# Performance work log

Measured on AMD Instinct MI355X. Metric: run time of the kernel, lower is better.

The kernel has to match this reference:

```python
import jax, jax.numpy as jnp
import numpy as np

# Video-DiT scale: d_model = H * D = 2048
B, S_T, S_C, H, D = 2, 2048, 1024, 16, 128


def setup_inputs() -> dict:
    key = jax.random.key(0)
    ks = jax.random.split(key, 6)
    f = lambda k, s: jax.random.normal(k, s, dtype=jnp.float32)
    return {
        "target_q": f(ks[0], (B, S_T, H, D)),
        "target_k": f(ks[1], (B, S_T, H, D)),
        "target_v": f(ks[2], (B, S_T, H, D)),
        "cond_k": f(ks[3], (B, S_C, H, D)),
        "cond_v": f(ks[4], (B, S_C, H, D)),
        "b_param": f(ks[5], (1,)),
    }


def reference(target_q, target_k, target_v, cond_k, cond_v, b_param):
    """Extended target self-attention over [target_k; cond_k] with a scalar
    logit bias b_param added only to the condition-key columns.
    Inputs BSHD; returns [B, S_t, H*D] (ready for output_proj)."""
    Bq, St, Hh, Dd = target_q.shape
    Sc = cond_k.shape[1]
    scale = Dd ** -0.5  # softmax_scale defaults to head_dim**-0.5

    k_ext = jnp.concatenate([target_k, cond_k], axis=1)  # [B, S_t+S_c, H, D]
    v_ext = jnp.concatenate([target_v, cond_v], axis=1)

    # [B, H, S_t, S_t+S_c]
    logits = jnp.einsum('bqhd,bkhd->bhqk', target_q, k_ext) * jnp.asarray(scale, target_q.dtype)
    # bias: 0 on target keys, b on cond keys
    bias = jnp.concatenate([
        jnp.zeros((St,), logits.dtype),
        jnp.broadcast_to(b_param.astype(logits.dtype), (Sc,)),
    ])
    logits = logits + bias[None, None, None, :]

    probs = jax.nn.softmax(logits, axis=-1)
    out = jnp.einsum('bhqk,bkhd->bqhd', probs, v_ext)  # [B, S_t, H, D]
    return out.reshape(Bq, St, Hh * Dd)
```

## Files before the change

### kernel.cpp

```cpp
#include <hip/hip_runtime.h>
#include <hip/hip_bf16.h>

typedef __attribute__((ext_vector_type(4))) float f32x4;
typedef __attribute__((ext_vector_type(16))) float f32x16;
typedef __attribute__((ext_vector_type(8))) short bf8;
typedef __attribute__((ext_vector_type(2))) int i32x2;

#define B_ 2
#define ST 2048
#define SC 1024
#define SK 3072
#define NH 16
#define DH 128
#define KVB 32
#define NT 96
#define TGT 64
#define SCALE 0.088388347648318447f
#define LOG2E 1.4426950408889634f
#define PRE_TILE_U32 2048
#define PRE_BYTES (32ull * 96 * 512 * 16)
#define WS_NEED (2ull * PRE_BYTES)

__device__ __forceinline__ i32x2 tr_read(unsigned a) {
    i32x2 d;
    asm volatile("ds_read_b64_tr_b16 %0, %1" : "=v"(d) : "v"(a));
    return d;
}

__device__ __forceinline__ unsigned cvtpk(float lo, float hi) {
    unsigned r;
    asm("v_cvt_pk_bf16_f32 %0, %1, %2" : "=v"(r) : "v"(lo), "v"(hi));
    return r;
}

__device__ __forceinline__ void swap32(unsigned &a, unsigned &b) {
    asm volatile("v_permlane32_swap_b32 %0, %1" : "+v"(a), "+v"(b));
}

__device__ __forceinline__ bf8 mk_bf8(i32x2 a, i32x2 b) {
    union { i32x2 h[2]; bf8 v; } u;
    u.h[0] = a; u.h[1] = b;
    return u.v;
}
__device__ __forceinline__ bf8 mk_bf8w(unsigned w0, unsigned w1, unsigned w2, unsigned w3) {
    union { unsigned w[4]; bf8 v; } u;
    u.w[0] = w0; u.w[1] = w1; u.w[2] = w2; u.w[3] = w3;
    return u.v;
}
__device__ __forceinline__ bf8 pack_bf8(f32x4 a, f32x4 b) {
    return mk_bf8w(cvtpk(a[0], a[1]), cvtpk(a[2], a[3]),
                   cvtpk(b[0], b[1]), cvtpk(b[2], b[3]));
}

__global__ __launch_bounds__(256)
void preconv(const float* __restrict__ TK, const float* __restrict__ TV,
             const float* __restrict__ CK, const float* __restrict__ CV,
             unsigned* __restrict__ KP, unsigned* __restrict__ VP)
{
    const unsigned gid = blockIdx.x * 256 + threadIdx.x;
    const int c    = gid & 511;
    const int idx  = gid >> 9;
    const int bhid = idx / 96;
    const int t    = idx - bhid * 96;
    const int bb   = bhid >> 4;
    const int hh   = bhid & 15;

    const int krow = c >> 4;
    const int kcol = ((c & 15) ^ (krow & 7)) << 3;
    const int gkv  = t * 32 + krow;
    const float* kp = (gkv < ST)
        ? TK + (((size_t)bb * ST + gkv) * NH + hh) * DH + kcol
        : CK + (((size_t)bb * SC + (gkv - ST)) * NH + hh) * DH + kcol;
    const f32x4 k0 = *(const f32x4*)kp;
    const f32x4 k1 = *(const f32x4*)(kp + 4);
    unsigned* ko = KP + (size_t)gid * 4;
    ko[0] = cvtpk(k0[0], k0[1]); ko[1] = cvtpk(k0[2], k0[3]);
    ko[2] = cvtpk(k1[0], k1[1]); ko[3] = cvtpk(k1[2], k1[3]);

    const int vkv = (((c >> 8) & 1) << 4) | (((c >> 4) & 1) << 3)
                  | (((c >> 7) & 1) << 2) | ((c >> 1) & 3);
    const int vd  = (((c >> 5) & 3) << 5) | (((c >> 3) & 1) << 4)
                  | ((c & 1) << 3);
    const int gvv = t * 32 + vkv;
    const float* vp = (gvv < ST)
        ? TV + (((size_t)bb * ST + gvv) * NH + hh) * DH + vd
        : CV + (((size_t)bb * SC + (gvv - ST)) * NH + hh) * DH + vd;
    const f32x4 v0 = *(const f32x4*)vp;
    const f32x4 v1 = *(const f32x4*)(vp + 4);
    unsigned* vo = VP + (size_t)gid * 4;
    vo[0] = cvtpk(v0[0], v0[1]); vo[1] = cvtpk(v0[2], v0[3]);
    vo[2] = cvtpk(v1[0], v1[1]); vo[3] = cvtpk(v1[2], v1[3]);
}

__global__ __launch_bounds__(256) __attribute__((amdgpu_waves_per_eu(2, 2)))
void attn_fwd_pre(const float* __restrict__ Q,
                  const unsigned* __restrict__ KP,
                  const unsigned* __restrict__ VP,
                  const float* __restrict__ BP,
                  float* __restrict__ OUT)
{
    __shared__ __align__(16) unsigned short Ks[3][KVB * DH];
    __shared__ __align__(16) unsigned short Vs[3][KVB * DH];

    const int tid = threadIdx.x;
    const int w   = tid >> 6;
    const int l   = tid & 63;
    const int r31 = l & 31;
    const int hi  = l >> 5;

    const int bid = blockIdx.x;
    const int xcd = bid & 7;
    const int sub = bid >> 3;
    const int bh  = xcd * 4 + (sub >> 4);
    const int qt  = sub & 15;
    const int bb  = bh >> 4;
    const int hh  = bh & 15;
    const int bh96 = bh * 96;

    const float biasl = BP[0] * LOG2E;

    const int qrow = qt * 128 + w * 32 + r31;
    const float* qp = Q + (((size_t)bb * ST + qrow) * NH + hh) * DH;
    const float qsc = SCALE * LOG2E;
    bf8 qf[8];
#pragma unroll
    for (int dk = 0; dk < 8; ++dk) {
        const f32x4 x0 = *(const f32x4*)(qp + dk * 16 + hi * 8);
        const f32x4 x1 = *(const f32x4*)(qp + dk * 16 + hi * 8 + 4);
        qf[dk] = mk_bf8w(cvtpk(x0[0]*qsc, x0[1]*qsc), cvtpk(x0[2]*qsc, x0[3]*qsc),
                         cvtpk(x1[0]*qsc, x1[1]*qsc), cvtpk(x1[2]*qsc, x1[3]*qsc));
    }

    f32x16 oa[4];
#pragma unroll
    for (int dt = 0; dt < 4; ++dt)
#pragma unroll
        for (int e = 0; e < 16; ++e) oa[dt][e] = 0.f;
    float l_run = 0.f;

    auto stage = [&](int t, int buf) {
        const unsigned* kt = KP + (size_t)(bh96 + t) * PRE_TILE_U32;
        const unsigned* vt = VP + (size_t)(bh96 + t) * PRE_TILE_U32;
#pragma unroll
        for (int i = 0; i < 2; ++i) {
            const int cb = (w << 6) + (i << 8);
            const unsigned kdst = (unsigned)(size_t)&Ks[buf][cb * 8];
            const unsigned vdst = (unsigned)(size_t)&Vs[buf][cb * 8];
            const unsigned* kg = kt + (size_t)(cb + l) * 4;
            const unsigned* vg = vt + (size_t)(cb + l) * 4;
            __builtin_amdgcn_global_load_lds(
                (const __attribute__((address_space(1))) unsigned*)(size_t)kg,
                (__attribute__((address_space(3))) unsigned*)(size_t)kdst, 16, 0, 0);
            __builtin_amdgcn_global_load_lds(
                (const __attribute__((address_space(1))) unsigned*)(size_t)vg,
                (__attribute__((address_space(3))) unsigned*)(size_t)vdst, 16, 0, 0);
        }
    };

    const unsigned vLane = (unsigned)(size_t)&Vs[0][0]
                         + (unsigned)((l >> 4) * 128 + (l & 15) * 8);
    const char* kBase = (const char*)Ks[0];

    auto qk_into = [&](f32x16& SN, int bufn, float biasn) {
#pragma unroll
        for (int e = 0; e < 16; ++e) SN[e] = biasn;
        const char* kB = kBase + (unsigned)bufn * 8192u;
        __builtin_amdgcn_s_setprio(1);
#pragma unroll
        for (int dk = 0; dk < 8; ++dk) {
            int o = r31 * 256 + (dk * 16 + hi * 8) * 2;
            o ^= (r31 & 7) << 4;
            const bf8 kf = *(const bf8*)(kB + o);
            SN = __builtin_amdgcn_mfma_f32_32x32x16_bf16(kf, qf[dk], SN, 0, 0, 0);
        }
        __builtin_amdgcn_s_setprio(0);
    };

    stage(0, 0);
    stage(1, 1);
    asm volatile("s_waitcnt vmcnt(4)" ::: "memory");
    __builtin_amdgcn_s_barrier();
    asm volatile("" ::: "memory");
    f32x16 sA, sB;
    qk_into(sA, 0, 0.f);

    int b0 = 0, b1 = 1, b2 = 2;

    auto body = [&](int t, f32x16& SCr, f32x16& SNr) {
        if (t + 1 < NT) asm volatile("s_waitcnt vmcnt(0)" ::: "memory");
        __builtin_amdgcn_s_barrier();
        asm volatile("" ::: "memory");
        if (t + 2 < NT) stage(t + 2, b2);

        if (t + 1 < NT)
            qk_into(SNr, b1, (t + 1 >= TGT) ? biasl : 0.f);

        const unsigned vA = vLane + (unsigned)b0 * 8192u;
        i32x2 t0_[4][2];
#pragma unroll
        for (int dt = 0; dt < 4; ++dt) {
            t0_[dt][0] = tr_read(vA + dt * 512);
            t0_[dt][1] = tr_read(vA + dt * 512 + 2048);
        }

        float rs = 0.f;
#pragma unroll
        for (int e = 0; e < 16; ++e) {
            SCr[e] = __builtin_amdgcn_exp2f(SCr[e]);
            rs += SCr[e];
        }
        l_run += rs;

        unsigned a0 = cvtpk(SCr[0], SCr[1]),  c0 = cvtpk(SCr[4], SCr[5]);
        unsigned a1 = cvtpk(SCr[2], SCr[3]),  c1 = cvtpk(SCr[6], SCr[7]);
        swap32(a0, c0); swap32(a1, c1);
        const bf8 pf0 = mk_bf8w(a0, a1, c0, c1);
        unsigned a2 = cvtpk(SCr[8], SCr[9]),   c2 = cvtpk(SCr[12], SCr[13]);
        unsigned a3 = cvtpk(SCr[10], SCr[11]), c3 = cvtpk(SCr[14], SCr[15]);
        swap32(a2, c2); swap32(a3, c3);
        const bf8 pf1 = mk_bf8w(a2, a3, c2, c3);

        asm volatile("s_waitcnt lgkmcnt(0)");
        __builtin_amdgcn_sched_barrier(0);
        i32x2 t1_[4][2];
#pragma unroll
        for (int dt = 0; dt < 4; ++dt) {
            t1_[dt][0] = tr_read(vA + 4096 + dt * 512);
            t1_[dt][1] = tr_read(vA + 4096 + dt * 512 + 2048);
        }
        __builtin_amdgcn_s_setprio(1);
#pragma unroll
        for (int dt = 0; dt < 4; ++dt) {
            const bf8 vf = mk_bf8(t0_[dt][0], t0_[dt][1]);
            oa[dt] = __builtin_amdgcn_mfma_f32_32x32x16_bf16(vf, pf0, oa[dt], 0, 0, 0);
        }
        __builtin_amdgcn_s_setprio(0);
        asm volatile("s_waitcnt lgkmcnt(0)");
        __builtin_amdgcn_sched_barrier(0);
        __builtin_amdgcn_s_setprio(1);
#pragma unroll
        for (int dt = 0; dt < 4; ++dt) {
            const bf8 vf = mk_bf8(t1_[dt][0], t1_[dt][1]);
            oa[dt] = __builtin_amdgcn_mfma_f32_32x32x16_bf16(vf, pf1, oa[dt], 0, 0, 0);
        }
        __builtin_amdgcn_s_setprio(0);

        const int n0 = b1, n1 = b2, n2 = b0;
        b0 = n0; b1 = n1; b2 = n2;
    };

    for (int t = 0; t < NT; t += 2) {
        body(t, sA, sB);
        body(t + 1, sB, sA);
    }

    const float l_tot = l_run + __shfl_xor(l_run, 32);
    const float inv = 1.0f / l_tot;
    float* op = OUT + ((size_t)(bb * ST + qrow)) * (NH * DH) + hh * DH;
#pragma unroll
    for (int dt = 0; dt < 4; ++dt)
#pragma unroll
        for (int rr = 0; rr < 4; ++rr) {
            f32x4 st;
            st[0] = oa[dt][rr * 4 + 0] * inv;
            st[1] = oa[dt][rr * 4 + 1] * inv;
            st[2] = oa[dt][rr * 4 + 2] * inv;
            st[3] = oa[dt][rr * 4 + 3] * inv;
            *(f32x4*)(op + dt * 32 + rr * 8 + hi * 4) = st;
        }
}

__global__ __launch_bounds__(256, 2)
void attn_fwd_reg(const float* __restrict__ Q,
                  const float* __restrict__ TK,
                  const float* __restrict__ TV,
                  const float* __restrict__ CK,
                  const float* __restrict__ CV,
                  const float* __restrict__ BP,
                  float* __restrict__ OUT)
{
    __shared__ __align__(16) unsigned short Ks[2][KVB * DH];
    __shared__ __align__(16) unsigned short Vs[2][KVB * DH];

    const int tid = threadIdx.x;
    const int w   = tid >> 6;
    const int l   = tid & 63;
    const int r31 = l & 31;
    const int hi  = l >> 5;

    const int bid = blockIdx.x;
    const int xcd = bid & 7;
    const int sub = bid >> 3;
    const int bh  = xcd * 4 + (sub >> 4);
    const int qt  = sub & 15;
    const int bb  = bh >> 4;
    const int hh  = bh & 15;

    const float biasl = BP[0] * LOG2E;

    const int qrow = qt * 128 + w * 32 + r31;
    const float* qp = Q + (((size_t)bb * ST + qrow) * NH + hh) * DH;
    const float qsc = SCALE * LOG2E;
    bf8 qf[8];
#pragma unroll
    for (int dk = 0; dk < 8; ++dk) {
        const f32x4 x0 = *(const f32x4*)(qp + dk * 16 + hi * 8);
        const f32x4 x1 = *(const f32x4*)(qp + dk * 16 + hi * 8 + 4);
        qf[dk] = mk_bf8w(cvtpk(x0[0]*qsc, x0[1]*qsc), cvtpk(x0[2]*qsc, x0[3]*qsc),
                         cvtpk(x1[0]*qsc, x1[1]*qsc), cvtpk(x1[2]*qsc, x1[3]*qsc));
    }

    f32x16 oa[4];
#pragma unroll
    for (int dt = 0; dt < 4; ++dt)
#pragma unroll
        for (int e = 0; e < 16; ++e) oa[dt][e] = 0.f;
    float l_run = 0.f;

    f32x4 skr[2][2], svr[2][2];

    auto stage_load = [&](int t) {
        const int kv0 = t * KVB;
        const float *kb, *vb;
        if (kv0 < ST) {
            const size_t off = (((size_t)bb * ST + kv0) * NH + hh) * DH;
            kb = TK + off; vb = TV + off;
        } else {
            const size_t off = (((size_t)bb * SC + (kv0 - ST)) * NH + hh) * DH;
            kb = CK + off; vb = CV + off;
        }
#pragma unroll
        for (int i = 0; i < 2; ++i) {
            const int c = tid + (i << 8);
            const int krow = c >> 4;
            const int kcol = ((c & 15) ^ (krow & 7)) << 3;
            const float* kp = kb + (size_t)krow * (NH * DH) + kcol;
            skr[i][0] = *(const f32x4*)kp;
            skr[i][1] = *(const f32x4*)(kp + 4);
            const int vkv = (((c >> 8) & 1) << 4) | (((c >> 4) & 1) << 3)
                          | (((c >> 7) & 1) << 2) | ((c >> 1) & 3);
            const int vd  = (((c >> 5) & 3) << 5) | (((c >> 3) & 1) << 4)
                          | ((c & 1) << 3);
            const float* vp = vb + (size_t)vkv * (NH * DH) + vd;
            svr[i][0] = *(const f32x4*)vp;
            svr[i][1] = *(const f32x4*)(vp + 4);
        }
    };
    auto stage_write = [&](int buf) {
#pragma unroll
        for (int i = 0; i < 2; ++i) {
            const int c = tid + (i << 8);
            *(bf8*)((char*)Ks[buf] + c * 16) = pack_bf8(skr[i][0], skr[i][1]);
            *(bf8*)((char*)Vs[buf] + c * 16) = pack_bf8(svr[i][0], svr[i][1]);
        }
    };

    stage_load(0);
    stage_write(0);

    const unsigned vLane = (unsigned)(size_t)&Vs[0][0]
                         + (unsigned)((l >> 4) * 128 + (l & 15) * 8);

    for (int t = 0; t < NT; ++t) {
        __syncthreads();
        if (t + 1 < NT) stage_load(t + 1);
        const int buf = t & 1;
        const float bias = (t >= TGT) ? biasl : 0.f;

        f32x16 s0;
#pragma unroll
        for (int e = 0; e < 16; ++e) s0[e] = bias;
        __builtin_amdgcn_s_setprio(1);
#pragma unroll
        for (int dk = 0; dk < 8; ++dk) {
            int o = r31 * 256 + (dk * 16 + hi * 8) * 2;
            o ^= (r31 & 7) << 4;
            const bf8 kf = *(const bf8*)((const char*)Ks[buf] + o);
            s0 = __builtin_amdgcn_mfma_f32_32x32x16_bf16(kf, qf[dk], s0, 0, 0, 0);
        }
        __builtin_amdgcn_s_setprio(0);

        asm volatile("" ::: "memory");
        const unsigned vA = vLane + (unsigned)(buf << 13);
        i32x2 vt_[2][4][2];
#pragma unroll
        for (int ks = 0; ks < 2; ++ks) {
            const unsigned vk = vA + (unsigned)(ks << 12);
#pragma unroll
            for (int dt = 0; dt < 4; ++dt) {
                vt_[ks][dt][0] = tr_read(vk + dt * 512);
                vt_[ks][dt][1] = tr_read(vk + dt * 512 + 2048);
            }
        }

        if (t + 1 < NT) stage_write(buf ^ 1);

        float rs = 0.f;
#pragma unroll
        for (int e = 0; e < 16; ++e) {
            s0[e] = __builtin_amdgcn_exp2f(s0[e]);
            rs += s0[e];
        }
        l_run += rs;

        unsigned a0 = cvtpk(s0[0], s0[1]),  b0 = cvtpk(s0[4], s0[5]);
        unsigned a1 = cvtpk(s0[2], s0[3]),  b1 = cvtpk(s0[6], s0[7]);
        swap32(a0, b0); swap32(a1, b1);
        const bf8 pf0 = mk_bf8w(a0, a1, b0, b1);
        unsigned a2 = cvtpk(s0[8], s0[9]),   b2 = cvtpk(s0[12], s0[13]);
        unsigned a3 = cvtpk(s0[10], s0[11]), b3 = cvtpk(s0[14], s0[15]);
        swap32(a2, b2); swap32(a3, b3);
        const bf8 pf1 = mk_bf8w(a2, a3, b2, b3);

        asm volatile("s_waitcnt lgkmcnt(0)");
        __builtin_amdgcn_sched_barrier(0);
        __builtin_amdgcn_s_setprio(1);
#pragma unroll
        for (int ks = 0; ks < 2; ++ks) {
            const bf8 pf = ks ? pf1 : pf0;
#pragma unroll
            for (int dt = 0; dt < 4; ++dt) {
                const bf8 vf = mk_bf8(vt_[ks][dt][0], vt_[ks][dt][1]);
                oa[dt] = __builtin_amdgcn_mfma_f32_32x32x16_bf16(vf, pf, oa[dt], 0, 0, 0);
            }
        }
        __builtin_amdgcn_s_setprio(0);
    }

    const float l_tot = l_run + __shfl_xor(l_run, 32);
    const float inv = 1.0f / l_tot;
    float* op = OUT + ((size_t)(bb * ST + qrow)) * (NH * DH) + hh * DH;
#pragma unroll
    for (int dt = 0; dt < 4; ++dt)
#pragma unroll
        for (int rr = 0; rr < 4; ++rr) {
            f32x4 st;
            st[0] = oa[dt][rr * 4 + 0] * inv;
            st[1] = oa[dt][rr * 4 + 1] * inv;
            st[2] = oa[dt][rr * 4 + 2] * inv;
            st[3] = oa[dt][rr * 4 + 3] * inv;
            *(f32x4*)(op + dt * 32 + rr * 8 + hi * 4) = st;
        }
}

extern "C" void kernel_launch(void* const* d_in, const int* in_sizes, int n_in,
                              void* d_out, int out_size, void* d_ws, size_t ws_size,
                              hipStream_t stream) {
    const float* q  = (const float*)d_in[0];
    const float* tk = (const float*)d_in[1];
    const float* tv = (const float*)d_in[2];
    const float* ck = (const float*)d_in[3];
    const float* cv = (const float*)d_in[4];
    const float* bp = (const float*)d_in[5];
    float* out = (float*)d_out;

    if (ws_size >= WS_NEED) {
        unsigned* kp = (unsigned*)d_ws;
        unsigned* vp = (unsigned*)((char*)d_ws + PRE_BYTES);
        preconv<<<dim3(6144), 256, 0, stream>>>(tk, tv, ck, cv, kp, vp);
        attn_fwd_pre<<<dim3(512), 256, 0, stream>>>(q, kp, vp, bp, out);
    } else {
        attn_fwd_reg<<<dim3(512), 256, 0, stream>>>(q, tk, tv, ck, cv, bp, out);
    }
}
```

Baseline: 142.4 us.

## Pre-permute K/V tiles into per-lane MFMA fragment order for linear LDS reads

The preconversion kernel now writes K and V bf16 tiles already arranged in the exact per-lane MFMA operand order, so the attention kernel reads each fragment with a single contiguous 16-byte LDS load at lane*16 plus a fixed stride. This replaces the XOR-swizzled K addressing and the transposing ds_read_tr V loads, along with the interleaved waitcnt and sched_barrier staging. The cost is a strided scalar gather of V in preconv, eight separate column reads per thread instead of vectorized loads. The compiler also now schedules all eight V fragment loads itself.

```diff
diff --git a/kernel.cpp b/kernel.cpp
--- a/kernel.cpp
+++ b/kernel.cpp
@@ -64,32 +64,40 @@
     const int t    = idx - bhid * 96;
     const int bb   = bhid >> 4;
     const int hh   = bhid & 15;
-
-    const int krow = c >> 4;
-    const int kcol = ((c & 15) ^ (krow & 7)) << 3;
-    const int gkv  = t * 32 + krow;
-    const float* kp = (gkv < ST)
-        ? TK + (((size_t)bb * ST + gkv) * NH + hh) * DH + kcol
-        : CK + (((size_t)bb * SC + (gkv - ST)) * NH + hh) * DH + kcol;
-    const f32x4 k0 = *(const f32x4*)kp;
-    const f32x4 k1 = *(const f32x4*)(kp + 4);
-    unsigned* ko = KP + (size_t)gid * 4;
-    ko[0] = cvtpk(k0[0], k0[1]); ko[1] = cvtpk(k0[2], k0[3]);
-    ko[2] = cvtpk(k1[0], k1[1]); ko[3] = cvtpk(k1[2], k1[3]);
-
-    const int vkv = (((c >> 8) & 1) << 4) | (((c >> 4) & 1) << 3)
-                  | (((c >> 7) & 1) << 2) | ((c >> 1) & 3);
-    const int vd  = (((c >> 5) & 3) << 5) | (((c >> 3) & 1) << 4)
-                  | ((c & 1) << 3);
-    const int gvv = t * 32 + vkv;
-    const float* vp = (gvv < ST)
-        ? TV + (((size_t)bb * ST + gvv) * NH + hh) * DH + vd
-        : CV + (((size_t)bb * SC + (gvv - ST)) * NH + hh) * DH + vd;
-    const f32x4 v0 = *(const f32x4*)vp;
-    const f32x4 v1 = *(const f32x4*)(vp + 4);
-    unsigned* vo = VP + (size_t)gid * 4;
-    vo[0] = cvtpk(v0[0], v0[1]); vo[1] = cvtpk(v0[2], v0[3]);
-    vo[2] = cvtpk(v1[0], v1[1]); vo[3] = cvtpk(v1[2], v1[3]);
+    const int lc   = c & 63;
+    const int r31c = lc & 31;
+    const int hic  = lc >> 5;
+
+    const bool tgt = (t < TGT);
+    const size_t krowbase = tgt
+        ? (((size_t)bb * ST + t * 32) * NH + hh) * DH
+        : (((size_t)bb * SC + (t * 32 - ST)) * NH + hh) * DH;
+    const float* kb = (tgt ? TK : CK) + krowbase;
+    const float* vb = (tgt ? TV : CV) + krowbase;
+
+    {
+        const int dk = c >> 6;
+        const float* kp = kb + (size_t)r31c * (NH * DH) + dk * 16 + hic * 8;
+        const f32x4 k0 = *(const f32x4*)kp;
+        const f32x4 k1 = *(const f32x4*)(kp + 4);
+        unsigned* ko = KP + (size_t)gid * 4;
+        ko[0] = cvtpk(k0[0], k0[1]); ko[1] = cvtpk(k0[2], k0[3]);
+        ko[2] = cvtpk(k1[0], k1[1]); ko[3] = cvtpk(k1[2], k1[3]);
+    }
+
+    {
+        const int s  = c >> 6;
+        const int ks = s >> 2;
+        const int dt = s & 3;
+        const int d  = dt * 32 + r31c;
+        const float* vp = vb + (size_t)(ks * 16 + hic * 8) * (NH * DH) + d;
+        float vv[8];
+#pragma unroll
+        for (int j = 0; j < 8; ++j) vv[j] = vp[(size_t)j * (NH * DH)];
+        unsigned* vo = VP + (size_t)gid * 4;
+        vo[0] = cvtpk(vv[0], vv[1]); vo[1] = cvtpk(vv[2], vv[3]);
+        vo[2] = cvtpk(vv[4], vv[5]); vo[3] = cvtpk(vv[6], vv[7]);
+    }
 }
 
 __global__ __launch_bounds__(256) __attribute__((amdgpu_waves_per_eu(2, 2)))
@@ -157,20 +165,17 @@
         }
     };
 
-    const unsigned vLane = (unsigned)(size_t)&Vs[0][0]
-                         + (unsigned)((l >> 4) * 128 + (l & 15) * 8);
-    const char* kBase = (const char*)Ks[0];
+    const char* kLane = (const char*)&Ks[0][0] + l * 16;
+    const char* vLane = (const char*)&Vs[0][0] + l * 16;
 
     auto qk_into = [&](f32x16& SN, int bufn, float biasn) {
 #pragma unroll
         for (int e = 0; e < 16; ++e) SN[e] = biasn;
-        const char* kB = kBase + (unsigned)bufn * 8192u;
+        const char* kB = kLane + (unsigned)bufn * 8192u;
         __builtin_amdgcn_s_setprio(1);
 #pragma unroll
         for (int dk = 0; dk < 8; ++dk) {
-            int o = r31 * 256 + (dk * 16 + hi * 8) * 2;
-            o ^= (r31 & 7) << 4;
-            const bf8 kf = *(const bf8*)(kB + o);
+            const bf8 kf = *(const bf8*)(kB + dk * 1024);
             SN = __builtin_amdgcn_mfma_f32_32x32x16_bf16(kf, qf[dk], SN, 0, 0, 0);
         }
         __builtin_amdgcn_s_setprio(0);
@@ -195,13 +200,11 @@
         if (t + 1 < NT)
             qk_into(SNr, b1, (t + 1 >= TGT) ? biasl : 0.f);
 
-        const unsigned vA = vLane + (unsigned)b0 * 8192u;
-        i32x2 t0_[4][2];
-#pragma unroll
-        for (int dt = 0; dt < 4; ++dt) {
-            t0_[dt][0] = tr_read(vA + dt * 512);
-            t0_[dt][1] = tr_read(vA + dt * 512 + 2048);
-        }
+        const char* vB = vLane + (unsigned)b0 * 8192u;
+        bf8 vf[8];
+#pragma unroll
+        for (int s = 0; s < 8; ++s)
+            vf[s] = *(const bf8*)(vB + s * 1024);
 
         float rs = 0.f;
 #pragma unroll
@@ -220,29 +223,13 @@
         swap32(a2, c2); swap32(a3, c3);
         const bf8 pf1 = mk_bf8w(a2, a3, c2, c3);
 
-        asm volatile("s_waitcnt lgkmcnt(0)");
-        __builtin_amdgcn_sched_barrier(0);
-        i32x2 t1_[4][2];
-#pragma unroll
-        for (int dt = 0; dt < 4; ++dt) {
-            t1_[dt][0] = tr_read(vA + 4096 + dt * 512);
-            t1_[dt][1] = tr_read(vA + 4096 + dt * 512 + 2048);
-        }
         __builtin_amdgcn_s_setprio(1);
 #pragma unroll
-        for (int dt = 0; dt < 4; ++dt) {
-            const bf8 vf = mk_bf8(t0_[dt][0], t0_[dt][1]);
-            oa[dt] = __builtin_amdgcn_mfma_f32_32x32x16_bf16(vf, pf0, oa[dt], 0, 0, 0);
-        }
-        __builtin_amdgcn_s_setprio(0);
-        asm volatile("s_waitcnt lgkmcnt(0)");
-        __builtin_amdgcn_sched_barrier(0);
-        __builtin_amdgcn_s_setprio(1);
-#pragma unroll
-        for (int dt = 0; dt < 4; ++dt) {
-            const bf8 vf = mk_bf8(t1_[dt][0], t1_[dt][1]);
-            oa[dt] = __builtin_amdgcn_mfma_f32_32x32x16_bf16(vf, pf1, oa[dt], 0, 0, 0);
-        }
+        for (int dt = 0; dt < 4; ++dt)
+            oa[dt] = __builtin_amdgcn_mfma_f32_32x32x16_bf16(vf[dt], pf0, oa[dt], 0, 0, 0);
+#pragma unroll
+        for (int dt = 0; dt < 4; ++dt)
+            oa[dt] = __builtin_amdgcn_mfma_f32_32x32x16_bf16(vf[4 + dt], pf1, oa[dt], 0, 0, 0);
         __builtin_amdgcn_s_setprio(0);
 
         const int n0 = b1, n1 = b2, n2 = b0;
```

After: 139.0 us (median of 2 runs). 1.02x faster.
